# Kernel optimization log

Hardware: AMD Instinct MI355X
Metric: run time of the kernel (lower is better)

Reference implementation:

```python
import jax, jax.numpy as jnp
import numpy as np

B, S, D = 64, 2048, 512


def setup_inputs() -> dict:
    key = jax.random.key(0)
    ks = jax.random.split(key, 7)
    return {
        "c_i_1": jax.random.normal(ks[0], (B, D), dtype=jnp.float32),
        "q": jax.random.normal(ks[1], (B, D), dtype=jnp.float32),
        "cw_s": jax.random.normal(ks[2], (B, S, D), dtype=jnp.float32),
        "W_d2d": jax.random.normal(ks[3], (D, 2 * D), dtype=jnp.float32) * 0.02,
        "b_d": jax.random.normal(ks[4], (D,), dtype=jnp.float32) * 0.02,
        "W_1d": jax.random.normal(ks[5], (1, D), dtype=jnp.float32) * 0.02,
        "b_1": jax.random.normal(ks[6], (1,), dtype=jnp.float32) * 0.02,
    }


def reference(c_i_1, q, cw_s, W_d2d, b_d, W_1d, b_1):
    # concat previous control with question rep: [B, 2D]
    conc_cq = jnp.concatenate([c_i_1, q], axis=1)
    # small GEMM + bias: [B, D]
    cq_i = conc_cq @ W_d2d.T + b_d
    # broadcast multiply against contextual word states: [B, S, D]
    cqcw = cw_s * cq_i[:, None, :]
    # projection to attention logits: [B, S, 1]
    ca_is = jnp.einsum("bsd,od->bso", cqcw, W_1d) + b_1
    # attention over the sequence axis
    cv_is = jax.nn.softmax(ca_is, axis=1)
    # weighted sum -> new control state [B, D]
    c_i = jnp.sum(cv_is * cw_s, axis=1)
    return c_i
```

## Files before the change

kernel.cpp:

```cpp
#include <hip/hip_runtime.h>
#include <math.h>

#define BB 64
#define SS 2048
#define DD 512
#define CH 16
#define ROWS (SS/CH)
#define WROWS (ROWS/4)
#define RPI 4
#define ITERS (WROWS/RPI)

__global__ __launch_bounds__(128) void k_w(
    const float* __restrict__ c1, const float* __restrict__ q,
    const float* __restrict__ Wd, const float* __restrict__ bd,
    const float* __restrict__ W1, float* __restrict__ w)
{
    __shared__ float conc[2*DD];
    const int b = blockIdx.y;
    const int t = threadIdx.x;
    for (int i = t; i < DD; i += 128) {
        conc[i]      = c1[b*DD + i];
        conc[DD + i] = q[b*DD + i];
    }
    __syncthreads();
    const int d = blockIdx.x * 128 + t;
    const float4* Wr = (const float4*)(Wd + (size_t)d * (2*DD));
    const float4* cc = (const float4*)conc;
    float acc = 0.f;
    #pragma unroll 8
    for (int k = 0; k < (2*DD)/4; ++k) {
        float4 a = Wr[k];
        float4 c = cc[k];
        acc += a.x*c.x + a.y*c.y + a.z*c.z + a.w*c.w;
    }
    w[b*DD + d] = (acc + bd[d]) * W1[d];
}

__global__ __launch_bounds__(256) void k_pass(
    const float* __restrict__ cw, const float* __restrict__ w,
    float* __restrict__ pm, float* __restrict__ pl, float* __restrict__ pacc)
{
    const int blk  = blockIdx.x;
    const int b    = blk >> 4;
    const int ch   = blk & (CH - 1);
    const int tid  = threadIdx.x;
    const int wave = tid >> 6;
    const int lane = tid & 63;

    const float4* wb = (const float4*)(w + b*DD);
    const float4 w0 = wb[lane];
    const float4 w1 = wb[64 + lane];

    const float* rb = cw + ((size_t)b*SS + (size_t)ch*ROWS + (size_t)wave*WROWS) * DD;

    float4 c0[RPI], c1v[RPI];
    #pragma unroll
    for (int r = 0; r < RPI; ++r) {
        const float4* p = (const float4*)(rb + (size_t)r * DD);
        c0[r]  = p[lane];
        c1v[r] = p[64 + lane];
    }

    float m = -INFINITY, l = 0.f;
    float4 a0 = make_float4(0,0,0,0), a1 = make_float4(0,0,0,0);

    #pragma unroll 2
    for (int i = 0; i < ITERS; ++i) {
        const int nx = (i + 1 < ITERS) ? (i + 1) : i;
        const float* nbase = rb + (size_t)nx * RPI * DD;
        float4 n0[RPI], n1[RPI];
        #pragma unroll
        for (int r = 0; r < RPI; ++r) {
            const float4* p = (const float4*)(nbase + (size_t)r * DD);
            n0[r] = p[lane];
            n1[r] = p[64 + lane];
        }

        float d_[RPI];
        #pragma unroll
        for (int r = 0; r < RPI; ++r) {
            d_[r] = c0[r].x*w0.x + c0[r].y*w0.y + c0[r].z*w0.z + c0[r].w*w0.w
                  + c1v[r].x*w1.x + c1v[r].y*w1.y + c1v[r].z*w1.z + c1v[r].w*w1.w;
        }
        #pragma unroll
        for (int off = 32; off; off >>= 1) {
            #pragma unroll
            for (int r = 0; r < RPI; ++r) d_[r] += __shfl_xor(d_[r], off, 64);
        }

        float mn = fmaxf(fmaxf(d_[0], d_[1]), fmaxf(d_[2], d_[3]));
        mn = fmaxf(mn, m);
        const float alpha = __expf(m - mn);
        m = mn;
        float pr[RPI];
        #pragma unroll
        for (int r = 0; r < RPI; ++r) pr[r] = __expf(d_[r] - m);
        l = l*alpha + (pr[0] + pr[1] + pr[2] + pr[3]);
        a0.x *= alpha; a0.y *= alpha; a0.z *= alpha; a0.w *= alpha;
        a1.x *= alpha; a1.y *= alpha; a1.z *= alpha; a1.w *= alpha;
        #pragma unroll
        for (int r = 0; r < RPI; ++r) {
            a0.x += pr[r]*c0[r].x;  a0.y += pr[r]*c0[r].y;
            a0.z += pr[r]*c0[r].z;  a0.w += pr[r]*c0[r].w;
            a1.x += pr[r]*c1v[r].x; a1.y += pr[r]*c1v[r].y;
            a1.z += pr[r]*c1v[r].z; a1.w += pr[r]*c1v[r].w;
        }

        #pragma unroll
        for (int r = 0; r < RPI; ++r) { c0[r] = n0[r]; c1v[r] = n1[r]; }
    }

    __shared__ float lm[4], ll[4];
    __shared__ float lacc[4][DD];
    if (lane == 0) lm[wave] = m;
    __syncthreads();
    const float M = fmaxf(fmaxf(lm[0], lm[1]), fmaxf(lm[2], lm[3]));
    const float beta = __expf(m - M);
    float4* lw = (float4*)lacc[wave];
    lw[lane]      = make_float4(a0.x*beta, a0.y*beta, a0.z*beta, a0.w*beta);
    lw[64 + lane] = make_float4(a1.x*beta, a1.y*beta, a1.z*beta, a1.w*beta);
    if (lane == 0) ll[wave] = l * beta;
    __syncthreads();
    const float s0 = lacc[0][tid]     + lacc[1][tid]     + lacc[2][tid]     + lacc[3][tid];
    const float s1 = lacc[0][tid+256] + lacc[1][tid+256] + lacc[2][tid+256] + lacc[3][tid+256];
    pacc[(size_t)blk*DD + tid]       = s0;
    pacc[(size_t)blk*DD + tid + 256] = s1;
    if (tid == 0) {
        pm[blk] = M;
        pl[blk] = ll[0] + ll[1] + ll[2] + ll[3];
    }
}

__global__ __launch_bounds__(256) void k_comb(
    const float* __restrict__ pm, const float* __restrict__ pl,
    const float* __restrict__ pacc, float* __restrict__ out)
{
    const int b = blockIdx.x;
    const int tid = threadIdx.x;
    float M = -INFINITY;
    #pragma unroll
    for (int p = 0; p < CH; ++p) M = fmaxf(M, pm[b*CH + p]);
    float L = 0.f;
    float sx = 0.f, sy = 0.f;
    #pragma unroll
    for (int p = 0; p < CH; ++p) {
        const float sc = __expf(pm[b*CH + p] - M);
        L += pl[b*CH + p] * sc;
        const float2 v = ((const float2*)(pacc + (size_t)(b*CH + p)*DD))[tid];
        sx += sc * v.x;
        sy += sc * v.y;
    }
    const float inv = 1.f / L;
    ((float2*)(out + b*DD))[tid] = make_float2(sx*inv, sy*inv);
}

extern "C" void kernel_launch(void* const* d_in, const int* in_sizes, int n_in,
                              void* d_out, int out_size, void* d_ws, size_t ws_size,
                              hipStream_t stream)
{
    const float* c1 = (const float*)d_in[0];
    const float* q  = (const float*)d_in[1];
    const float* cw = (const float*)d_in[2];
    const float* Wd = (const float*)d_in[3];
    const float* bd = (const float*)d_in[4];
    const float* W1 = (const float*)d_in[5];

    float* out  = (float*)d_out;
    float* ws   = (float*)d_ws;
    float* w    = ws;
    float* pm   = w  + BB*DD;
    float* pl   = pm + BB*CH;
    float* pacc = pl + BB*CH;

    k_w   <<<dim3(DD/128, BB), 128, 0, stream>>>(c1, q, Wd, bd, W1, w);
    k_pass<<<BB*CH,            256, 0, stream>>>(cw, w, pm, pl, pacc);
    k_comb<<<BB,               256, 0, stream>>>(pm, pl, pacc, out);
}
```

Baseline: 405.3 us.

## Split sequence into more chunks, fully unroll row loop, drop manual prefetch

Doubles the number of sequence chunks per batch, giving twice as many blocks with half the rows each, and halves rows per iteration. The manual double-buffered register prefetch is replaced by a fully unrolled loop so the compiler can schedule the loads itself, and a launch-bounds occupancy hint of 6 blocks per CU is added. The aim is more waves in flight to hide HBM latency on the streaming pass over cw_s, at the cost of more partial results to write and combine and some register pressure from full unrolling.

Result: slower. 455.7 us (+12.4%).

```diff
diff --git a/kernel.cpp b/kernel.cpp
--- a/kernel.cpp
+++ b/kernel.cpp
@@ -4,10 +4,10 @@
 #define BB 64
 #define SS 2048
 #define DD 512
-#define CH 16
+#define CH 32
 #define ROWS (SS/CH)
 #define WROWS (ROWS/4)
-#define RPI 4
+#define RPI 2
 #define ITERS (WROWS/RPI)
 
 __global__ __launch_bounds__(128) void k_w(
@@ -36,12 +36,12 @@
     w[b*DD + d] = (acc + bd[d]) * W1[d];
 }
 
-__global__ __launch_bounds__(256) void k_pass(
+__global__ __launch_bounds__(256, 6) void k_pass(
     const float* __restrict__ cw, const float* __restrict__ w,
     float* __restrict__ pm, float* __restrict__ pl, float* __restrict__ pacc)
 {
     const int blk  = blockIdx.x;
-    const int b    = blk >> 4;
+    const int b    = blk >> 5;
     const int ch   = blk & (CH - 1);
     const int tid  = threadIdx.x;
     const int wave = tid >> 6;
@@ -53,27 +53,17 @@
 
     const float* rb = cw + ((size_t)b*SS + (size_t)ch*ROWS + (size_t)wave*WROWS) * DD;
 
-    float4 c0[RPI], c1v[RPI];
-    #pragma unroll
-    for (int r = 0; r < RPI; ++r) {
-        const float4* p = (const float4*)(rb + (size_t)r * DD);
-        c0[r]  = p[lane];
-        c1v[r] = p[64 + lane];
-    }
-
     float m = -INFINITY, l = 0.f;
     float4 a0 = make_float4(0,0,0,0), a1 = make_float4(0,0,0,0);
 
-    #pragma unroll 2
+    #pragma unroll
     for (int i = 0; i < ITERS; ++i) {
-        const int nx = (i + 1 < ITERS) ? (i + 1) : i;
-        const float* nbase = rb + (size_t)nx * RPI * DD;
-        float4 n0[RPI], n1[RPI];
+        float4 c0[RPI], c1v[RPI];
         #pragma unroll
         for (int r = 0; r < RPI; ++r) {
-            const float4* p = (const float4*)(nbase + (size_t)r * DD);
-            n0[r] = p[lane];
-            n1[r] = p[64 + lane];
+            const float4* p = (const float4*)(rb + (size_t)(i*RPI + r) * DD);
+            c0[r]  = p[lane];
+            c1v[r] = p[64 + lane];
         }
 
         float d_[RPI];
@@ -88,26 +78,20 @@
             for (int r = 0; r < RPI; ++r) d_[r] += __shfl_xor(d_[r], off, 64);
         }
 
-        float mn = fmaxf(fmaxf(d_[0], d_[1]), fmaxf(d_[2], d_[3]));
-        mn = fmaxf(mn, m);
+        const float mn = fmaxf(fmaxf(d_[0], d_[1]), m);
         const float alpha = __expf(m - mn);
         m = mn;
-        float pr[RPI];
-        #pragma unroll
-        for (int r = 0; r < RPI; ++r) pr[r] = __expf(d_[r] - m);
-        l = l*alpha + (pr[0] + pr[1] + pr[2] + pr[3]);
-        a0.x *= alpha; a0.y *= alpha; a0.z *= alpha; a0.w *= alpha;
-        a1.x *= alpha; a1.y *= alpha; a1.z *= alpha; a1.w *= alpha;
-        #pragma unroll
-        for (int r = 0; r < RPI; ++r) {
-            a0.x += pr[r]*c0[r].x;  a0.y += pr[r]*c0[r].y;
-            a0.z += pr[r]*c0[r].z;  a0.w += pr[r]*c0[r].w;
-            a1.x += pr[r]*c1v[r].x; a1.y += pr[r]*c1v[r].y;
-            a1.z += pr[r]*c1v[r].z; a1.w += pr[r]*c1v[r].w;
-        }
-
-        #pragma unroll
-        for (int r = 0; r < RPI; ++r) { c0[r] = n0[r]; c1v[r] = n1[r]; }
+        const float p0 = __expf(d_[0] - m);
+        const float p1 = __expf(d_[1] - m);
+        l = l*alpha + p0 + p1;
+        a0.x = a0.x*alpha + p0*c0[0].x  + p1*c0[1].x;
+        a0.y = a0.y*alpha + p0*c0[0].y  + p1*c0[1].y;
+        a0.z = a0.z*alpha + p0*c0[0].z  + p1*c0[1].z;
+        a0.w = a0.w*alpha + p0*c0[0].w  + p1*c0[1].w;
+        a1.x = a1.x*alpha + p0*c1v[0].x + p1*c1v[1].x;
+        a1.y = a1.y*alpha + p0*c1v[0].y + p1*c1v[1].y;
+        a1.z = a1.z*alpha + p0*c1v[0].z + p1*c1v[1].z;
+        a1.w = a1.w*alpha + p0*c1v[0].w + p1*c1v[1].w;
     }
 
     __shared__ float lm[4], ll[4];
```
